# Performance work log

Measured on AMD Instinct MI355X. Metric: run time of the kernel, lower is better.

Reference implementation:

```python
import jax, jax.numpy as jnp
import numpy as np

CL = 256   # context_length (global in original code)
IL = 64    # inst_length (global in original code)
PC, CH1, CH2, CH3 = 64, 128, 256, 256
CK1, CK2, CK3 = 3, 3, 3
CS1, CS2, CS3 = 1, 2, 2
CP1, CP2, CP3 = 1, 1, 1
BCH1, BCH2, BCH3 = 64, 128, 256
F1, OUT = 1024, 2
B = 2048
C3_OUT = 64 * CH3            # 16384, per __init__ formula with CL-1=255
F1_IN = C3_OUT + BCH3        # 16640


def _conv1d(x, W, b, stride, pad):
    # x: [B, Cin, L], W: [Cout, Cin, K]
    y = jax.lax.conv_general_dilated(x, W, window_strides=(stride,),
                                     padding=[(pad, pad)],
                                     dimension_numbers=("NCH", "OIH", "NCH"))
    return y + b[None, :, None]


def setup_inputs() -> dict:
    key = jax.random.key(0)
    ks = jax.random.split(key, 20)
    s = lambda *sh: 1.0 / np.sqrt(np.prod(sh[1:]))
    def w(k, *sh):
        return jax.random.normal(k, sh, dtype=jnp.float32) * s(*sh)
    return {
        "x": jax.random.normal(ks[0], (B, CL * IL), dtype=jnp.float32),
        "Wp": w(ks[1], PC, IL, 2), "bp": jnp.zeros((PC,), jnp.float32),
        "W1": w(ks[2], CH1, PC, CK1), "b1": jnp.zeros((CH1,), jnp.float32),
        "W2": w(ks[3], CH2, CH1, CK2), "b2": jnp.zeros((CH2,), jnp.float32),
        "W3": w(ks[4], CH3, CH2, CK3), "b3": jnp.zeros((CH3,), jnp.float32),
        "Wb1": w(ks[5], BCH1, IL), "bb1": jnp.zeros((BCH1,), jnp.float32),
        "Wb2": w(ks[6], BCH2, BCH1), "bb2": jnp.zeros((BCH2,), jnp.float32),
        "Wb3": w(ks[7], BCH3, BCH2), "bb3": jnp.zeros((BCH3,), jnp.float32),
        "Wfc1": w(ks[8], F1, F1_IN), "bfc1": jnp.zeros((F1,), jnp.float32),
        "Wfc2": w(ks[9], OUT, F1), "bfc2": jnp.zeros((OUT,), jnp.float32),
    }


def reference(x, Wp, bp, W1, b1, W2, b2, W3, b3,
              Wb1, bb1, Wb2, bb2, Wb3, bb3, Wfc1, bfc1, Wfc2, bfc2):
    xr = x.reshape(-1, CL, IL).transpose(0, 2, 1)   # [B, IL, CL]
    x0 = xr[:, :, 0]                                 # [B, IL]
    # Fused replacement for the convp loop: kernel-2 conv over (x0, x_i)
    # y[:, :, i-1] = Wp[:,:,0] @ x0 + Wp[:,:,1] @ x_i + bp
    y = (jnp.einsum("bi,pi->bp", x0, Wp[:, :, 0])[:, :, None]
         + jnp.einsum("bic,pi->bpc", xr[:, :, 1:], Wp[:, :, 1])
         + bp[None, :, None])                        # [B, PC, CL-1]
    # bypass path on the first instruction (kernel-size-1 convs == matmuls)
    f = jax.nn.relu(x0 @ Wb1.T + bb1)
    f = jax.nn.relu(f @ Wb2.T + bb2)
    f = jax.nn.relu(f @ Wb3.T + bb3)                 # [B, BCH3]
    h = jax.nn.relu(y)
    h = jax.nn.relu(_conv1d(h, W1, b1, CS1, CP1))
    h = jax.nn.relu(_conv1d(h, W2, b2, CS2, CP2))
    h = jax.nn.relu(_conv1d(h, W3, b3, CS3, CP3))    # [B, CH3, 64]
    h = h.reshape(h.shape[0], C3_OUT)
    z = jnp.concatenate([h, f], axis=1)              # [B, F1_IN]
    z = jax.nn.relu(z @ Wfc1.T + bfc1)
    return z @ Wfc2.T + bfc2                         # [B, OUT]
```

## Files before the change

kernel.cpp:

```cpp
#include <hip/hip_runtime.h>
#include <cstdint>
#include <cstddef>

typedef __attribute__((ext_vector_type(8))) short bf16x8;
typedef __attribute__((ext_vector_type(8))) unsigned short ushort8;
typedef __attribute__((ext_vector_type(4))) float f32x4;

__device__ __forceinline__ unsigned short f2bf(float f){
  unsigned int u = __float_as_uint(f);
  unsigned int lsb = (u >> 16) & 1u;
  u += 0x7fffu + lsb;
  return (unsigned short)(u >> 16);
}

__device__ __forceinline__ void gload16(const void* g, void* l){
  __builtin_amdgcn_global_load_lds(
      (const __attribute__((address_space(1))) unsigned int*)g,
      (__attribute__((address_space(3))) unsigned int*)l, 16, 0, 0);
}

__global__ __launch_bounds__(256) void pack_w_bf16_kernel(const float* __restrict__ W,
                                                          unsigned short* __restrict__ Wb,
                                                          int COUT, int CIN){
  int idx = blockIdx.x*256 + threadIdx.x;
  int tot = COUT*CIN*3;
  if (idx >= tot) return;
  int o = idx/(CIN*3); int r = idx - o*(CIN*3); int kk = r/CIN; int ci = r - kk*CIN;
  Wb[idx] = f2bf(W[(o*CIN + ci)*3 + kk]);
}

__global__ __launch_bounds__(256) void pack_wp_kernel(const float* __restrict__ Wp,
                                                      unsigned short* __restrict__ Bw){
  int idx = blockIdx.x*256 + threadIdx.x;
  if (idx >= 64*128) return;
  int p = idx >> 7, k = idx & 127;
  float v = (k < 64) ? Wp[p*128 + k*2] : Wp[p*128 + (k-64)*2 + 1];
  Bw[idx] = f2bf(v);
}

__global__ __launch_bounds__(256) void f2bf_kernel(const float* __restrict__ src,
                                                   unsigned short* __restrict__ dst, int n){
  int i = blockIdx.x*256 + threadIdx.x;
  if (i < n) dst[i] = f2bf(src[i]);
}

__global__ __launch_bounds__(256) void branch_kernel(const float* __restrict__ x,
    const float* __restrict__ Wb1, const float* __restrict__ bb1,
    const float* __restrict__ Wb2, const float* __restrict__ bb2,
    const float* __restrict__ Wb3, const float* __restrict__ bb3,
    unsigned short* __restrict__ Hcat){
  __shared__ float s0[64], s1[64], s2[128];
  const int b = blockIdx.x, tid = threadIdx.x;
  const float* xb = x + (size_t)b*16384;
  if (tid < 64) s0[tid] = xb[tid];
  __syncthreads();
  if (tid < 64){
    float a = bb1[tid];
    for (int k=0;k<64;k++) a = fmaf(Wb1[tid*64+k], s0[k], a);
    s1[tid] = fmaxf(a, 0.f);
  }
  __syncthreads();
  if (tid < 128){
    float a = bb2[tid];
    for (int k=0;k<64;k++) a = fmaf(Wb2[tid*64+k], s1[k], a);
    s2[tid] = fmaxf(a, 0.f);
  }
  __syncthreads();
  float a = bb3[tid];
  for (int k=0;k<128;k++) a = fmaf(Wb3[tid*128+k], s2[k], a);
  Hcat[(size_t)b*16640 + 16384 + tid] = f2bf(fmaxf(a, 0.f));
}

__global__ __launch_bounds__(256) void h0_gemm_kernel(const float* __restrict__ x,
    const unsigned short* __restrict__ Bw, const float* __restrict__ bp,
    unsigned short* __restrict__ h0o){
  __shared__ __align__(16) char sAraw[128*256];
  __shared__ __align__(16) char sBraw[64*256];
  const int tid = threadIdx.x;
  const int m0 = blockIdx.x*128;
  #pragma unroll
  for (int i=0;i<16;i++){
    int j = tid + 256*i;
    int row = j >> 5, q = j & 31;
    int m = m0 + row;
    int b = m / 255, c = m - b*255;
    const float* xb = x + (size_t)b*16384;
    int k = q*4;
    const float* src = (k < 64) ? (xb + k) : (xb + (c+1)*64 + (k-64));
    float4 v = *(const float4*)src;
    ushort4 u; u.x=f2bf(v.x); u.y=f2bf(v.y); u.z=f2bf(v.z); u.w=f2bf(v.w);
    *(ushort4*)(sAraw + row*256 + ((k*2) ^ ((row&7)<<4))) = u;
  }
  #pragma unroll
  for (int i=0;i<4;i++){
    int j = tid + 256*i;
    int row = j >> 4, q = j & 15;
    int k = q*8;
    ushort8 u = *(const ushort8*)(Bw + row*128 + k);
    *(ushort8*)(sBraw + row*256 + ((k*2) ^ ((row&7)<<4))) = u;
  }
  __syncthreads();
  const int lane = tid & 63, wid = tid >> 6;
  const int lr = lane & 15, lg = lane >> 4;
  f32x4 zero = {0.f,0.f,0.f,0.f};
  f32x4 acc[2][4];
  #pragma unroll
  for (int a=0;a<2;a++){ acc[a][0]=zero; acc[a][1]=zero; acc[a][2]=zero; acc[a][3]=zero; }
  #pragma unroll
  for (int ks=0; ks<4; ks++){
    int k = ks*32 + lg*8;
    bf16x8 af[2], bfr[4];
    #pragma unroll
    for (int f=0; f<2; f++){
      int row = wid*32 + f*16 + lr;
      af[f] = *(const bf16x8*)(sAraw + row*256 + ((k*2) ^ ((row&7)<<4)));
    }
    #pragma unroll
    for (int f=0; f<4; f++){
      int row = f*16 + lr;
      bfr[f] = *(const bf16x8*)(sBraw + row*256 + ((k*2) ^ ((row&7)<<4)));
    }
    #pragma unroll
    for (int fi=0; fi<2; fi++)
      #pragma unroll
      for (int fj=0; fj<4; fj++)
        acc[fi][fj] = __builtin_amdgcn_mfma_f32_16x16x32_bf16(af[fi], bfr[fj], acc[fi][fj], 0,0,0);
  }
  #pragma unroll
  for (int fi=0; fi<2; fi++)
    #pragma unroll
    for (int fj=0; fj<4; fj++)
      #pragma unroll
      for (int j=0;j<4;j++){
        int m = m0 + wid*32 + fi*16 + lg*4 + j;
        int n = fj*16 + lr;
        h0o[(size_t)m*64 + n] = f2bf(fmaxf(acc[fi][fj][j] + bp[n], 0.f));
      }
}

template<int CIN,int COUT,int S,int LIN,int LOUT,int BM,int BN,int WN,bool TO_HCAT>
__global__ __launch_bounds__(256) void conv_gemm_kernel(
    const unsigned short* __restrict__ in, const unsigned short* __restrict__ Wb,
    const float* __restrict__ bias, unsigned short* __restrict__ out){
  constexpr int MT = (LOUT + BM - 1)/BM;
  __shared__ __align__(16) char sA[BM*128];
  __shared__ __align__(16) char sB[BN*128];
  const int tid = threadIdx.x;
  const int b  = blockIdx.y;
  const int mt = blockIdx.x % MT;
  const int nt = blockIdx.x / MT;
  const int m0 = mt*BM, n0 = nt*BN;
  const unsigned short* inb = in + (size_t)b*LIN*CIN;
  const int lane = tid & 63, wid = tid >> 6;
  const int wm = wid / WN, wn = wid % WN;
  const int lr = lane & 15, lg = lane >> 4;
  f32x4 zero = {0.f,0.f,0.f,0.f};
  f32x4 acc[4][4];
  #pragma unroll
  for (int i=0;i<4;i++){ acc[i][0]=zero; acc[i][1]=zero; acc[i][2]=zero; acc[i][3]=zero; }
  #pragma unroll
  for (int kk=0; kk<3; kk++){
    #pragma unroll
    for (int cc=0; cc<CIN/64; cc++){
      __syncthreads();
      #pragma unroll
      for (int p=0; p<BM/32; p++){
        int slot = tid + p*256;
        int row = slot >> 3, c8 = slot & 7;
        int pos = (m0 + row)*S - 1 + kk;
        ushort8 v = {0,0,0,0,0,0,0,0};
        if (pos >= 0 && pos < LIN)
          v = *(const ushort8*)(inb + (size_t)pos*CIN + cc*64 + c8*8);
        *(ushort8*)(sA + row*128 + ((c8*16) ^ ((row&7)<<4))) = v;
      }
      #pragma unroll
      for (int p=0; p<BN/32; p++){
        int slot = tid + p*256;
        int row = slot >> 3, c8 = slot & 7;
        ushort8 v = *(const ushort8*)(Wb + ((size_t)(n0+row)*3 + kk)*CIN + cc*64 + c8*8);
        *(ushort8*)(sB + row*128 + ((c8*16) ^ ((row&7)<<4))) = v;
      }
      __syncthreads();
      #pragma unroll
      for (int ks=0; ks<2; ks++){
        const int k = ks*32 + lg*8;
        bf16x8 af[4], bf[4];
        #pragma unroll
        for (int f=0;f<4;f++){
          int ra = wm*64 + f*16 + lr;
          af[f] = *(const bf16x8*)(sA + ra*128 + ((k*2) ^ ((ra&7)<<4)));
          int rb = wn*64 + f*16 + lr;
          bf[f] = *(const bf16x8*)(sB + rb*128 + ((k*2) ^ ((rb&7)<<4)));
        }
        #pragma unroll
        for (int fi=0;fi<4;fi++)
          #pragma unroll
          for (int fj=0;fj<4;fj++)
            acc[fi][fj] = __builtin_amdgcn_mfma_f32_16x16x32_bf16(af[fi], bf[fj], acc[fi][fj], 0,0,0);
      }
    }
  }
  unsigned short* outb = TO_HCAT ? (out + (size_t)b*16640) : (out + (size_t)b*LOUT*COUT);
  #pragma unroll
  for (int fi=0;fi<4;fi++)
    #pragma unroll
    for (int fj=0;fj<4;fj++)
      #pragma unroll
      for (int j=0;j<4;j++){
        int m = m0 + wm*64 + fi*16 + lg*4 + j;
        int n = n0 + wn*64 + fj*16 + lr;
        if (m < LOUT){
          float val = fmaxf(acc[fi][fj][j] + bias[n], 0.f);
          if (TO_HCAT) outb[(size_t)n*64 + m] = f2bf(val);
          else         outb[(size_t)m*COUT + n] = f2bf(val);
        }
      }
}

__global__ __launch_bounds__(256) void fc1_gemm_kernel(
    const unsigned short* __restrict__ A, const unsigned short* __restrict__ Bw,
    float* __restrict__ zp, int zoffm, int MT, int KZ){
  __shared__ __align__(16) char sA[128*128];
  __shared__ __align__(16) char sB[128*128];
  const int tid = threadIdx.x;
  const int nwg = gridDim.x;
  const int lgid = (blockIdx.x % 8)*(nwg/8) + blockIdx.x/8;
  const int kz  = lgid / (8*MT);
  const int rem = lgid % (8*MT);
  const int nt  = rem / MT;
  const int mt  = rem % MT;
  const int n0 = nt*128, m0 = mt*128;
  const int lane = tid & 63, wid = tid >> 6;
  const int wm = wid >> 1, wn = wid & 1;
  const int lr = lane & 15, lg = lane >> 4;
  const int srow = lane >> 3;
  const int soff = (((lane&7) ^ srow) << 3);
  f32x4 zero = {0.f,0.f,0.f,0.f};
  f32x4 acc[4][4];
  #pragma unroll
  for (int i=0;i<4;i++){ acc[i][0]=zero; acc[i][1]=zero; acc[i][2]=zero; acc[i][3]=zero; }
  const int it0 = (kz*260)/KZ, it1 = ((kz+1)*260)/KZ;
  for (int it=it0; it<it1; ++it){
    const size_t k0 = (size_t)it*64;
    __syncthreads();
    #pragma unroll
    for (int s=0;s<4;s++){
      int row = wid*32 + s*8 + srow;
      gload16(A  + (size_t)(m0+row)*16640 + k0 + soff, sA + wid*4096 + s*1024);
      gload16(Bw + (size_t)(n0+row)*16640 + k0 + soff, sB + wid*4096 + s*1024);
    }
    __syncthreads();
    #pragma unroll
    for (int ks=0; ks<2; ks++){
      const int k = ks*32 + lg*8;
      bf16x8 af[4], bfr[4];
      #pragma unroll
      for (int f=0;f<4;f++){
        int rowa = wm*64 + f*16 + lr;
        af[f]  = *(const bf16x8*)(sA + rowa*128 + ((k*2) ^ ((rowa&7)<<4)));
        int rowb = wn*64 + f*16 + lr;
        bfr[f] = *(const bf16x8*)(sB + rowb*128 + ((k*2) ^ ((rowb&7)<<4)));
      }
      #pragma unroll
      for (int fi=0;fi<4;fi++)
        #pragma unroll
        for (int fj=0;fj<4;fj++)
          acc[fi][fj] = __builtin_amdgcn_mfma_f32_16x16x32_bf16(af[fi], bfr[fj], acc[fi][fj], 0,0,0);
    }
  }
  float* zo = zp + (size_t)kz*zoffm;
  #pragma unroll
  for (int fi=0;fi<4;fi++)
    #pragma unroll
    for (int fj=0;fj<4;fj++)
      #pragma unroll
      for (int j=0;j<4;j++){
        int m = m0 + wm*64 + fi*16 + lg*4 + j;
        int n = n0 + wn*64 + fj*16 + lr;
        zo[(size_t)m*1024 + n] = acc[fi][fj][j];
      }
}

__global__ __launch_bounds__(256) void fc2_kernel(const float* __restrict__ zp, int zoffm, int KZ,
    const float* __restrict__ bfc1, const float* __restrict__ Wfc2,
    const float* __restrict__ bfc2, float* __restrict__ out){
  __shared__ float red[4][2];
  const int b = blockIdx.x, tid = threadIdx.x;
  float a0 = 0.f, a1 = 0.f;
  for (int n = tid; n < 1024; n += 256){
    float s = bfc1[n];
    const float* zb = zp + (size_t)b*1024 + n;
    for (int kz = 0; kz < KZ; kz++) s += zb[(size_t)kz*zoffm];
    s = fmaxf(s, 0.f);
    a0 = fmaf(s, Wfc2[n], a0);
    a1 = fmaf(s, Wfc2[1024+n], a1);
  }
  #pragma unroll
  for (int m=32; m>=1; m>>=1){ a0 += __shfl_xor(a0, m, 64); a1 += __shfl_xor(a1, m, 64); }
  const int w = tid >> 6;
  if ((tid & 63) == 0){ red[w][0] = a0; red[w][1] = a1; }
  __syncthreads();
  if (tid == 0){
    float s0 = red[0][0]+red[1][0]+red[2][0]+red[3][0];
    float s1 = red[0][1]+red[1][1]+red[2][1]+red[3][1];
    out[(size_t)b*2]   = s0 + bfc2[0];
    out[(size_t)b*2+1] = s1 + bfc2[1];
  }
}

extern "C" void kernel_launch(void* const* d_in, const int* in_sizes, int n_in,
                              void* d_out, int out_size, void* d_ws, size_t ws_size,
                              hipStream_t stream){
  const float* x    = (const float*)d_in[0];
  const float* Wp   = (const float*)d_in[1];
  const float* bp   = (const float*)d_in[2];
  const float* W1   = (const float*)d_in[3];
  const float* b1   = (const float*)d_in[4];
  const float* W2   = (const float*)d_in[5];
  const float* b2   = (const float*)d_in[6];
  const float* W3   = (const float*)d_in[7];
  const float* b3   = (const float*)d_in[8];
  const float* Wb1  = (const float*)d_in[9];
  const float* bb1  = (const float*)d_in[10];
  const float* Wb2  = (const float*)d_in[11];
  const float* bb2  = (const float*)d_in[12];
  const float* Wb3  = (const float*)d_in[13];
  const float* bb3  = (const float*)d_in[14];
  const float* Wfc1 = (const float*)d_in[15];
  const float* bfc1 = (const float*)d_in[16];
  const float* Wfc2 = (const float*)d_in[17];
  const float* bfc2 = (const float*)d_in[18];
  float* out = (float*)d_out;

  size_t off = 0;
  char* basep = (char*)d_ws;
  auto carve = [&](size_t bytes)->char*{
    char* q = basep + off; off += (bytes + 255) & ~(size_t)255; return q;
  };
  unsigned short* W1b   = (unsigned short*)carve((size_t)128*3*64*2);
  unsigned short* W2b   = (unsigned short*)carve((size_t)256*3*128*2);
  unsigned short* W3b   = (unsigned short*)carve((size_t)256*3*256*2);
  unsigned short* Bwp   = (unsigned short*)carve((size_t)64*128*2);
  unsigned short* Wfc1b = (unsigned short*)carve((size_t)1024*16640*2);
  size_t fixed = off;

  int Bc = 128, KZ = 64;
  {
    const int bcs[5] = {2048, 1024, 512, 256, 128};
    const int kzs[5] = {4, 8, 16, 32, 64};
    for (int i = 0; i < 5; i++){
      size_t b = bcs[i];
      size_t need = fixed + b*((size_t)65536+65280+33280) + (size_t)kzs[i]*b*4096 + 16*256;
      if (need <= ws_size){ Bc = bcs[i]; KZ = kzs[i]; break; }
    }
  }
  const int NC = 2048/Bc;
  const int MT = Bc/128;
  unsigned short* buf1 = (unsigned short*)carve((size_t)Bc*65536);
  unsigned short* buf2 = (unsigned short*)carve((size_t)Bc*65280);
  unsigned short* Hcat = (unsigned short*)carve((size_t)Bc*33280);
  float*          zp   = (float*)carve((size_t)KZ*Bc*4096);
  const int zoffm = Bc*1024;

  hipLaunchKernelGGL(pack_w_bf16_kernel, dim3((128*64*3+255)/256), dim3(256), 0, stream, W1, W1b, 128, 64);
  hipLaunchKernelGGL(pack_w_bf16_kernel, dim3((256*128*3+255)/256), dim3(256), 0, stream, W2, W2b, 256, 128);
  hipLaunchKernelGGL(pack_w_bf16_kernel, dim3((256*256*3+255)/256), dim3(256), 0, stream, W3, W3b, 256, 256);
  hipLaunchKernelGGL(pack_wp_kernel, dim3(32), dim3(256), 0, stream, Wp, Bwp);
  hipLaunchKernelGGL(f2bf_kernel, dim3((17039360+255)/256), dim3(256), 0, stream, Wfc1, Wfc1b, 17039360);

  for (int c = 0; c < NC; ++c){
    const float* xc = x + (size_t)c*Bc*16384;
    hipLaunchKernelGGL(branch_kernel, dim3(Bc), dim3(256), 0, stream,
                       xc, Wb1, bb1, Wb2, bb2, Wb3, bb3, Hcat);
    hipLaunchKernelGGL(h0_gemm_kernel, dim3(Bc*255/128), dim3(256), 0, stream, xc, Bwp, bp, buf1);
    hipLaunchKernelGGL((conv_gemm_kernel<64,128,1,255,255,128,128,2,false>), dim3(2, Bc), dim3(256), 0, stream,
                       buf1, W1b, b1, buf2);
    hipLaunchKernelGGL((conv_gemm_kernel<128,256,2,255,128,128,128,2,false>), dim3(2, Bc), dim3(256), 0, stream,
                       buf2, W2b, b2, buf1);
    hipLaunchKernelGGL((conv_gemm_kernel<256,256,2,128,64,64,256,4,true>), dim3(1, Bc), dim3(256), 0, stream,
                       buf1, W3b, b3, Hcat);
    hipLaunchKernelGGL(fc1_gemm_kernel, dim3(8*MT*KZ), dim3(256), 0, stream,
                       Hcat, Wfc1b, zp, zoffm, MT, KZ);
    hipLaunchKernelGGL(fc2_kernel, dim3(Bc), dim3(256), 0, stream,
                       zp, zoffm, KZ, bfc1, Wfc2, bfc2, out + (size_t)c*Bc*2);
  }
}
```

Measured before the change: 668.8 us.

## Pad conv activations with zero guard rows and flatten batch into GEMM M

Activation buffers gain a zero row before and after each sample, filled by a new guard-zeroing kernel, so the conv im2col loads need no bounds checks. The conv GEMM now treats batch times length as one M dimension with fixed 128x128 tiles. It stages tiles with direct global-to-LDS 16-byte loads, which removes register staging and lets tiles span sample boundaries so M=255 is no longer wasted on padding. In exchange it adds extra small kernel launches and slightly larger buffers, and it depends on the K ordering of the packed weights matching contiguous im2col rows.

```diff
diff --git a/kernel.cpp b/kernel.cpp
--- a/kernel.cpp
+++ b/kernel.cpp
@@ -42,6 +42,17 @@
                                                    unsigned short* __restrict__ dst, int n){
   int i = blockIdx.x*256 + threadIdx.x;
   if (i < n) dst[i] = f2bf(src[i]);
+}
+
+__global__ __launch_bounds__(256) void zero_guards_kernel(unsigned short* __restrict__ buf,
+                                                          int LINP, int CIN, int nb){
+  int idx = blockIdx.x*256 + threadIdx.x;
+  int per = 2*CIN/8;
+  if (idx >= nb*per) return;
+  int b = idx / per, r = idx - b*per;
+  int g = r / (CIN/8), c8 = r - g*(CIN/8);
+  ushort8 z = {0,0,0,0,0,0,0,0};
+  *(ushort8*)(buf + ((size_t)b*LINP + (size_t)g*(LINP-1))*CIN + c8*8) = z;
 }
 
 __global__ __launch_bounds__(256) void branch_kernel(const float* __restrict__ x,
@@ -134,73 +145,68 @@
       for (int j=0;j<4;j++){
         int m = m0 + wid*32 + fi*16 + lg*4 + j;
         int n = fj*16 + lr;
-        h0o[(size_t)m*64 + n] = f2bf(fmaxf(acc[fi][fj][j] + bp[n], 0.f));
-      }
-}
-
-template<int CIN,int COUT,int S,int LIN,int LOUT,int BM,int BN,int WN,bool TO_HCAT>
+        int b = m / 255, t = m - b*255;
+        h0o[((size_t)b*257 + t + 1)*64 + n] = f2bf(fmaxf(acc[fi][fj][j] + bp[n], 0.f));
+      }
+}
+
+template<int CIN,int COUT,int S,int LINP,int LOUT,bool TO_HCAT>
 __global__ __launch_bounds__(256) void conv_gemm_kernel(
     const unsigned short* __restrict__ in, const unsigned short* __restrict__ Wb,
     const float* __restrict__ bias, unsigned short* __restrict__ out){
-  constexpr int MT = (LOUT + BM - 1)/BM;
-  __shared__ __align__(16) char sA[BM*128];
-  __shared__ __align__(16) char sB[BN*128];
+  constexpr int K = 3*CIN;
+  constexpr int KS = K/64;
+  __shared__ __align__(16) char sA[128*128];
+  __shared__ __align__(16) char sB[128*128];
   const int tid = threadIdx.x;
-  const int b  = blockIdx.y;
-  const int mt = blockIdx.x % MT;
-  const int nt = blockIdx.x / MT;
-  const int m0 = mt*BM, n0 = nt*BN;
-  const unsigned short* inb = in + (size_t)b*LIN*CIN;
+  const int m0 = blockIdx.x*128;
+  const int n0 = blockIdx.y*128;
   const int lane = tid & 63, wid = tid >> 6;
-  const int wm = wid / WN, wn = wid % WN;
+  const int wm = wid >> 1, wn = wid & 1;
   const int lr = lane & 15, lg = lane >> 4;
+  const int srow = lane >> 3;
+  const int soff = (((lane&7) ^ srow) << 3);
+  const unsigned short* abase[4];
+  const unsigned short* bbase[4];
+  #pragma unroll
+  for (int s=0;s<4;s++){
+    int row = wid*32 + s*8 + srow;
+    int m = m0 + row;
+    int b = m / LOUT, t = m - b*LOUT;
+    abase[s] = in + ((size_t)b*LINP + (size_t)t*S)*CIN + soff;
+    bbase[s] = Wb + (size_t)(n0+row)*K + soff;
+  }
   f32x4 zero = {0.f,0.f,0.f,0.f};
   f32x4 acc[4][4];
   #pragma unroll
   for (int i=0;i<4;i++){ acc[i][0]=zero; acc[i][1]=zero; acc[i][2]=zero; acc[i][3]=zero; }
-  #pragma unroll
-  for (int kk=0; kk<3; kk++){
-    #pragma unroll
-    for (int cc=0; cc<CIN/64; cc++){
-      __syncthreads();
-      #pragma unroll
-      for (int p=0; p<BM/32; p++){
-        int slot = tid + p*256;
-        int row = slot >> 3, c8 = slot & 7;
-        int pos = (m0 + row)*S - 1 + kk;
-        ushort8 v = {0,0,0,0,0,0,0,0};
-        if (pos >= 0 && pos < LIN)
-          v = *(const ushort8*)(inb + (size_t)pos*CIN + cc*64 + c8*8);
-        *(ushort8*)(sA + row*128 + ((c8*16) ^ ((row&7)<<4))) = v;
-      }
-      #pragma unroll
-      for (int p=0; p<BN/32; p++){
-        int slot = tid + p*256;
-        int row = slot >> 3, c8 = slot & 7;
-        ushort8 v = *(const ushort8*)(Wb + ((size_t)(n0+row)*3 + kk)*CIN + cc*64 + c8*8);
-        *(ushort8*)(sB + row*128 + ((c8*16) ^ ((row&7)<<4))) = v;
-      }
-      __syncthreads();
-      #pragma unroll
-      for (int ks=0; ks<2; ks++){
-        const int k = ks*32 + lg*8;
-        bf16x8 af[4], bf[4];
+  for (int ks=0; ks<KS; ks++){
+    const int k0 = ks*64;
+    __syncthreads();
+    #pragma unroll
+    for (int s=0;s<4;s++){
+      gload16(abase[s] + k0, sA + wid*4096 + s*1024);
+      gload16(bbase[s] + k0, sB + wid*4096 + s*1024);
+    }
+    __syncthreads();
+    #pragma unroll
+    for (int kss=0; kss<2; kss++){
+      const int k = kss*32 + lg*8;
+      bf16x8 af[4], bfr[4];
+      #pragma unroll
+      for (int f=0;f<4;f++){
+        int ra = wm*64 + f*16 + lr;
+        af[f]  = *(const bf16x8*)(sA + ra*128 + ((k*2) ^ ((ra&7)<<4)));
+        int rb = wn*64 + f*16 + lr;
+        bfr[f] = *(const bf16x8*)(sB + rb*128 + ((k*2) ^ ((rb&7)<<4)));
+      }
+      #pragma unroll
+      for (int fi=0;fi<4;fi++)
         #pragma unroll
-        for (int f=0;f<4;f++){
-          int ra = wm*64 + f*16 + lr;
-          af[f] = *(const bf16x8*)(sA + ra*128 + ((k*2) ^ ((ra&7)<<4)));
-          int rb = wn*64 + f*16 + lr;
-          bf[f] = *(const bf16x8*)(sB + rb*128 + ((k*2) ^ ((rb&7)<<4)));
-        }
-        #pragma unroll
-        for (int fi=0;fi<4;fi++)
-          #pragma unroll
-          for (int fj=0;fj<4;fj++)
-            acc[fi][fj] = __builtin_amdgcn_mfma_f32_16x16x32_bf16(af[fi], bf[fj], acc[fi][fj], 0,0,0);
-      }
-    }
-  }
-  unsigned short* outb = TO_HCAT ? (out + (size_t)b*16640) : (out + (size_t)b*LOUT*COUT);
+        for (int fj=0;fj<4;fj++)
+          acc[fi][fj] = __builtin_amdgcn_mfma_f32_16x16x32_bf16(af[fi], bfr[fj], acc[fi][fj], 0,0,0);
+    }
+  }
   #pragma unroll
   for (int fi=0;fi<4;fi++)
     #pragma unroll
@@ -209,11 +215,10 @@
       for (int j=0;j<4;j++){
         int m = m0 + wm*64 + fi*16 + lg*4 + j;
         int n = n0 + wn*64 + fj*16 + lr;
-        if (m < LOUT){
-          float val = fmaxf(acc[fi][fj][j] + bias[n], 0.f);
-          if (TO_HCAT) outb[(size_t)n*64 + m] = f2bf(val);
-          else         outb[(size_t)m*COUT + n] = f2bf(val);
-        }
+        int b = m / LOUT, t = m - b*LOUT;
+        float val = fmaxf(acc[fi][fj][j] + bias[n], 0.f);
+        if (TO_HCAT) out[(size_t)b*16640 + (size_t)n*64 + t] = f2bf(val);
+        else         out[((size_t)b*(LOUT+2) + t + 1)*COUT + n] = f2bf(val);
       }
 }
 
@@ -350,14 +355,14 @@
     const int kzs[5] = {4, 8, 16, 32, 64};
     for (int i = 0; i < 5; i++){
       size_t b = bcs[i];
-      size_t need = fixed + b*((size_t)65536+65280+33280) + (size_t)kzs[i]*b*4096 + 16*256;
+      size_t need = fixed + b*((size_t)66560+65792+33280) + (size_t)kzs[i]*b*4096 + 16*256;
       if (need <= ws_size){ Bc = bcs[i]; KZ = kzs[i]; break; }
     }
   }
   const int NC = 2048/Bc;
   const int MT = Bc/128;
-  unsigned short* buf1 = (unsigned short*)carve((size_t)Bc*65536);
-  unsigned short* buf2 = (unsigned short*)carve((size_t)Bc*65280);
+  unsigned short* buf1 = (unsigned short*)carve((size_t)Bc*66560);
+  unsigned short* buf2 = (unsigned short*)carve((size_t)Bc*65792);
   unsigned short* Hcat = (unsigned short*)carve((size_t)Bc*33280);
   float*          zp   = (float*)carve((size_t)KZ*Bc*4096);
   const int zoffm = Bc*1024;
@@ -370,14 +375,20 @@
 
   for (int c = 0; c < NC; ++c){
     const float* xc = x + (size_t)c*Bc*16384;
+    hipLaunchKernelGGL(zero_guards_kernel, dim3((Bc*2*64/8+255)/256), dim3(256), 0, stream,
+                       buf1, 257, 64, Bc);
+    hipLaunchKernelGGL(zero_guards_kernel, dim3((Bc*2*128/8+255)/256), dim3(256), 0, stream,
+                       buf2, 257, 128, Bc);
     hipLaunchKernelGGL(branch_kernel, dim3(Bc), dim3(256), 0, stream,
                        xc, Wb1, bb1, Wb2, bb2, Wb3, bb3, Hcat);
     hipLaunchKernelGGL(h0_gemm_kernel, dim3(Bc*255/128), dim3(256), 0, stream, xc, Bwp, bp, buf1);
-    hipLaunchKernelGGL((conv_gemm_kernel<64,128,1,255,255,128,128,2,false>), dim3(2, Bc), dim3(256), 0, stream,
+    hipLaunchKernelGGL((conv_gemm_kernel<64,128,1,257,255,false>), dim3(Bc*255/128, 1), dim3(256), 0, stream,
                        buf1, W1b, b1, buf2);
-    hipLaunchKernelGGL((conv_gemm_kernel<128,256,2,255,128,128,128,2,false>), dim3(2, Bc), dim3(256), 0, stream,
+    hipLaunchKernelGGL(zero_guards_kernel, dim3((Bc*2*256/8+255)/256), dim3(256), 0, stream,
+                       buf1, 130, 256, Bc);
+    hipLaunchKernelGGL((conv_gemm_kernel<128,256,2,257,128,false>), dim3(Bc, 2), dim3(256), 0, stream,
                        buf2, W2b, b2, buf1);
-    hipLaunchKernelGGL((conv_gemm_kernel<256,256,2,128,64,64,256,4,true>), dim3(1, Bc), dim3(256), 0, stream,
+    hipLaunchKernelGGL((conv_gemm_kernel<256,256,2,130,64,true>), dim3(Bc/2, 2), dim3(256), 0, stream,
                        buf1, W3b, b3, Hcat);
     hipLaunchKernelGGL(fc1_gemm_kernel, dim3(8*MT*KZ), dim3(256), 0, stream,
                        Hcat, Wfc1b, zp, zoffm, MT, KZ);
```

Result: faster. 554.8 us (-17.1%).

## Fuse conv stages into two per-sample LDS-resident kernels

Applied to the files above, without the earlier changes.

Replaces the h0 GEMM and three separate conv GEMM launches with two per-sample kernels. fused1 computes the projection conv and conv1 entirely in shared memory. It also factors out the x0 term into a per-sample bias, so the K dimension is halved. fused2 keeps conv1 output and conv2 output in LDS to compute conv2 and conv3, with register-prefetched weight tiles. This cuts global round-trips of intermediate activations and the number of launches. The cost is very large LDS footprints (~115KB and ~154KB), which limit occupancy to one block per CU, and weights are reloaded per sample.

```diff
diff --git a/kernel.cpp b/kernel.cpp
--- a/kernel.cpp
+++ b/kernel.cpp
@@ -13,6 +13,11 @@
   return (unsigned short)(u >> 16);
 }
 
+__device__ __forceinline__ ushort8 cvt8(const float4 a, const float4 b){
+  ushort8 u; u[0]=f2bf(a.x); u[1]=f2bf(a.y); u[2]=f2bf(a.z); u[3]=f2bf(a.w);
+  u[4]=f2bf(b.x); u[5]=f2bf(b.y); u[6]=f2bf(b.z); u[7]=f2bf(b.w); return u;
+}
+
 __device__ __forceinline__ void gload16(const void* g, void* l){
   __builtin_amdgcn_global_load_lds(
       (const __attribute__((address_space(1))) unsigned int*)g,
@@ -20,8 +25,7 @@
 }
 
 __global__ __launch_bounds__(256) void pack_w_bf16_kernel(const float* __restrict__ W,
-                                                          unsigned short* __restrict__ Wb,
-                                                          int COUT, int CIN){
+    unsigned short* __restrict__ Wb, int COUT, int CIN){
   int idx = blockIdx.x*256 + threadIdx.x;
   int tot = COUT*CIN*3;
   if (idx >= tot) return;
@@ -29,13 +33,12 @@
   Wb[idx] = f2bf(W[(o*CIN + ci)*3 + kk]);
 }
 
-__global__ __launch_bounds__(256) void pack_wp_kernel(const float* __restrict__ Wp,
-                                                      unsigned short* __restrict__ Bw){
+__global__ __launch_bounds__(256) void pack_bh_kernel(const float* __restrict__ Wp,
+                                                      unsigned short* __restrict__ Bh){
   int idx = blockIdx.x*256 + threadIdx.x;
-  if (idx >= 64*128) return;
-  int p = idx >> 7, k = idx & 127;
-  float v = (k < 64) ? Wp[p*128 + k*2] : Wp[p*128 + (k-64)*2 + 1];
-  Bw[idx] = f2bf(v);
+  if (idx >= 64*64) return;
+  int p = idx >> 6, i = idx & 63;
+  Bh[idx] = f2bf(Wp[p*128 + i*2 + 1]);
 }
 
 __global__ __launch_bounds__(256) void f2bf_kernel(const float* __restrict__ src,
@@ -71,150 +74,297 @@
   Hcat[(size_t)b*16640 + 16384 + tid] = f2bf(fmaxf(a, 0.f));
 }
 
-__global__ __launch_bounds__(256) void h0_gemm_kernel(const float* __restrict__ x,
-    const unsigned short* __restrict__ Bw, const float* __restrict__ bp,
-    unsigned short* __restrict__ h0o){
-  __shared__ __align__(16) char sAraw[128*256];
-  __shared__ __align__(16) char sBraw[64*256];
-  const int tid = threadIdx.x;
-  const int m0 = blockIdx.x*128;
-  #pragma unroll
-  for (int i=0;i<16;i++){
-    int j = tid + 256*i;
-    int row = j >> 5, q = j & 31;
-    int m = m0 + row;
-    int b = m / 255, c = m - b*255;
-    const float* xb = x + (size_t)b*16384;
-    int k = q*4;
-    const float* src = (k < 64) ? (xb + k) : (xb + (c+1)*64 + (k-64));
-    float4 v = *(const float4*)src;
-    ushort4 u; u.x=f2bf(v.x); u.y=f2bf(v.y); u.z=f2bf(v.z); u.w=f2bf(v.w);
-    *(ushort4*)(sAraw + row*256 + ((k*2) ^ ((row&7)<<4))) = u;
-  }
+__global__ __launch_bounds__(512) void fused1_kernel(
+    const float* __restrict__ x, const float* __restrict__ Wp, const float* __restrict__ bp,
+    const unsigned short* __restrict__ Bh, const unsigned short* __restrict__ W1b,
+    const float* __restrict__ b1, unsigned short* __restrict__ c1g){
+  __shared__ __align__(16) char S[115392];
+  constexpr int SX = 0;
+  constexpr int SH = 37008;
+  constexpr int SB = 74160;
+  constexpr int SW = 106928;
+  constexpr int SY = 115120;
+  const int b = blockIdx.x, tid = threadIdx.x;
+  const int lane = tid & 63, wv = tid >> 6;
+  const int lr = lane & 15, lg = lane >> 4;
+  const float* xg = x + (size_t)b*16384;
+
   #pragma unroll
   for (int i=0;i<4;i++){
-    int j = tid + 256*i;
-    int row = j >> 4, q = j & 15;
-    int k = q*8;
-    ushort8 u = *(const ushort8*)(Bw + row*128 + k);
-    *(ushort8*)(sBraw + row*256 + ((k*2) ^ ((row&7)<<4))) = u;
+    int s = tid + 512*i;
+    int row = s>>3, sl = s&7;
+    const float4* src = (const float4*)(xg + row*64 + sl*8);
+    *(ushort8*)(S + SX + row*144 + sl*16) = cvt8(src[0], src[1]);
+  }
+  { int row = tid>>3, sl = tid&7;
+    ushort8 u = *(const ushort8*)(Bh + row*64 + sl*8);
+    *(ushort8*)(S + SW + row*128 + ((sl*16)^((row&7)<<4))) = u; }
+  ushort8 z8 = {0,0,0,0,0,0,0,0};
+  if (tid < 9)        *(ushort8*)(S + SX + 256*144 + tid*16) = z8;
+  else if (tid < 18)  *(ushort8*)(S + SH + 0*144   + (tid-9)*16) = z8;
+  else if (tid < 27)  *(ushort8*)(S + SH + 257*144 + (tid-18)*16) = z8;
+  if (tid < 64){
+    float a = bp[tid];
+    const float* wr = Wp + tid*128;
+    #pragma unroll 8
+    for (int i=0;i<64;i++) a = fmaf(wr[2*i], xg[i], a);
+    *(float*)(S + SY + tid*4) = a;
   }
   __syncthreads();
-  const int lane = tid & 63, wid = tid >> 6;
-  const int lr = lane & 15, lg = lane >> 4;
-  f32x4 zero = {0.f,0.f,0.f,0.f};
-  f32x4 acc[2][4];
-  #pragma unroll
-  for (int a=0;a<2;a++){ acc[a][0]=zero; acc[a][1]=zero; acc[a][2]=zero; acc[a][3]=zero; }
-  #pragma unroll
-  for (int ks=0; ks<4; ks++){
-    int k = ks*32 + lg*8;
-    bf16x8 af[2], bfr[4];
-    #pragma unroll
-    for (int f=0; f<2; f++){
-      int row = wid*32 + f*16 + lr;
-      af[f] = *(const bf16x8*)(sAraw + row*256 + ((k*2) ^ ((row&7)<<4)));
-    }
-    #pragma unroll
-    for (int f=0; f<4; f++){
-      int row = f*16 + lr;
-      bfr[f] = *(const bf16x8*)(sBraw + row*256 + ((k*2) ^ ((row&7)<<4)));
-    }
-    #pragma unroll
-    for (int fi=0; fi<2; fi++)
-      #pragma unroll
-      for (int fj=0; fj<4; fj++)
-        acc[fi][fj] = __builtin_amdgcn_mfma_f32_16x16x32_bf16(af[fi], bfr[fj], acc[fi][fj], 0,0,0);
-  }
-  #pragma unroll
-  for (int fi=0; fi<2; fi++)
-    #pragma unroll
-    for (int fj=0; fj<4; fj++)
-      #pragma unroll
-      for (int j=0;j<4;j++){
-        int m = m0 + wid*32 + fi*16 + lg*4 + j;
-        int n = fj*16 + lr;
-        h0o[(size_t)m*64 + n] = f2bf(fmaxf(acc[fi][fj][j] + bp[n], 0.f));
+
+  {
+    const int wm = wv>>1, wn = wv&1;
+    f32x4 acc[4][2];
+    #pragma unroll
+    for (int i=0;i<4;i++){ acc[i][0]=(f32x4){0,0,0,0}; acc[i][1]=(f32x4){0,0,0,0}; }
+    #pragma unroll
+    for (int ks=0; ks<2; ks++){
+      int k = ks*32 + lg*8;
+      bf16x8 af[4], bf[2];
+      #pragma unroll
+      for (int f=0;f<4;f++){ int ar = wm*64 + f*16 + lr + 1;
+        af[f] = *(const bf16x8*)(S + SX + ar*144 + k*2); }
+      #pragma unroll
+      for (int f=0;f<2;f++){ int rb = wn*32 + f*16 + lr;
+        bf[f] = *(const bf16x8*)(S + SW + rb*128 + ((k*2)^((rb&7)<<4))); }
+      #pragma unroll
+      for (int i=0;i<4;i++)
+        #pragma unroll
+        for (int j=0;j<2;j++)
+          acc[i][j] = __builtin_amdgcn_mfma_f32_16x16x32_bf16(af[i], bf[j], acc[i][j], 0,0,0);
+    }
+    #pragma unroll
+    for (int fm=0;fm<4;fm++)
+      #pragma unroll
+      for (int fn=0;fn<2;fn++)
+        #pragma unroll
+        for (int j=0;j<4;j++){
+          int t = wm*64 + fm*16 + lg*4 + j;
+          int p = wn*32 + fn*16 + lr;
+          float v = acc[fm][fn][j] + *(const float*)(S + SY + p*4);
+          unsigned short o = (t < 255) ? f2bf(fmaxf(v, 0.f)) : (unsigned short)0;
+          *(unsigned short*)(S + SH + (t+1)*144 + p*2) = o;
+        }
+  }
+
+  {
+    const int soff = ((lane&7)^(lane>>3))<<3;
+    const int rbase = wv*8 + (lane>>3);
+    #pragma unroll
+    for (int s=0;s<2;s++)
+      gload16(W1b + (size_t)(s*64 + rbase)*192 + soff, S + SB + s*8192 + wv*1024);
+    __syncthreads();
+
+    const int wm = wv>>1, wn = wv&1;
+    f32x4 acc[4][4];
+    #pragma unroll
+    for (int i=0;i<4;i++)
+      #pragma unroll
+      for (int j=0;j<4;j++) acc[i][j] = (f32x4){0,0,0,0};
+    #pragma unroll
+    for (int c=0;c<3;c++){
+      int buf = c&1;
+      if (c<2){
+        #pragma unroll
+        for (int s=0;s<2;s++)
+          gload16(W1b + (size_t)(s*64 + rbase)*192 + (c+1)*64 + soff,
+                  S + SB + (buf^1)*16384 + s*8192 + wv*1024);
       }
-}
-
-template<int CIN,int COUT,int S,int LIN,int LOUT,int BM,int BN,int WN,bool TO_HCAT>
-__global__ __launch_bounds__(256) void conv_gemm_kernel(
-    const unsigned short* __restrict__ in, const unsigned short* __restrict__ Wb,
-    const float* __restrict__ bias, unsigned short* __restrict__ out){
-  constexpr int MT = (LOUT + BM - 1)/BM;
-  __shared__ __align__(16) char sA[BM*128];
-  __shared__ __align__(16) char sB[BN*128];
-  const int tid = threadIdx.x;
-  const int b  = blockIdx.y;
-  const int mt = blockIdx.x % MT;
-  const int nt = blockIdx.x / MT;
-  const int m0 = mt*BM, n0 = nt*BN;
-  const unsigned short* inb = in + (size_t)b*LIN*CIN;
-  const int lane = tid & 63, wid = tid >> 6;
-  const int wm = wid / WN, wn = wid % WN;
-  const int lr = lane & 15, lg = lane >> 4;
-  f32x4 zero = {0.f,0.f,0.f,0.f};
-  f32x4 acc[4][4];
-  #pragma unroll
-  for (int i=0;i<4;i++){ acc[i][0]=zero; acc[i][1]=zero; acc[i][2]=zero; acc[i][3]=zero; }
-  #pragma unroll
-  for (int kk=0; kk<3; kk++){
-    #pragma unroll
-    for (int cc=0; cc<CIN/64; cc++){
-      __syncthreads();
-      #pragma unroll
-      for (int p=0; p<BM/32; p++){
-        int slot = tid + p*256;
-        int row = slot >> 3, c8 = slot & 7;
-        int pos = (m0 + row)*S - 1 + kk;
-        ushort8 v = {0,0,0,0,0,0,0,0};
-        if (pos >= 0 && pos < LIN)
-          v = *(const ushort8*)(inb + (size_t)pos*CIN + cc*64 + c8*8);
-        *(ushort8*)(sA + row*128 + ((c8*16) ^ ((row&7)<<4))) = v;
-      }
-      #pragma unroll
-      for (int p=0; p<BN/32; p++){
-        int slot = tid + p*256;
-        int row = slot >> 3, c8 = slot & 7;
-        ushort8 v = *(const ushort8*)(Wb + ((size_t)(n0+row)*3 + kk)*CIN + cc*64 + c8*8);
-        *(ushort8*)(sB + row*128 + ((c8*16) ^ ((row&7)<<4))) = v;
+      #pragma unroll
+      for (int ks=0; ks<2; ks++){
+        int k = ks*32 + lg*8;
+        bf16x8 af[4], bf[4];
+        #pragma unroll
+        for (int f=0;f<4;f++){ int ar = wm*64 + f*16 + lr + c;
+          af[f] = *(const bf16x8*)(S + SH + ar*144 + k*2); }
+        #pragma unroll
+        for (int f=0;f<4;f++){ int rb = wn*64 + f*16 + lr;
+          bf[f] = *(const bf16x8*)(S + SB + buf*16384 + rb*128 + ((k*2)^((rb&7)<<4))); }
+        #pragma unroll
+        for (int i=0;i<4;i++)
+          #pragma unroll
+          for (int j=0;j<4;j++)
+            acc[i][j] = __builtin_amdgcn_mfma_f32_16x16x32_bf16(af[i], bf[j], acc[i][j], 0,0,0);
       }
       __syncthreads();
-      #pragma unroll
-      for (int ks=0; ks<2; ks++){
-        const int k = ks*32 + lg*8;
-        bf16x8 af[4], bf[4];
-        #pragma unroll
-        for (int f=0;f<4;f++){
-          int ra = wm*64 + f*16 + lr;
-          af[f] = *(const bf16x8*)(sA + ra*128 + ((k*2) ^ ((ra&7)<<4)));
-          int rb = wn*64 + f*16 + lr;
-          bf[f] = *(const bf16x8*)(sB + rb*128 + ((k*2) ^ ((rb&7)<<4)));
+    }
+    unsigned short* cbo = c1g + (size_t)b*32640;
+    #pragma unroll
+    for (int fi=0;fi<4;fi++)
+      #pragma unroll
+      for (int fj=0;fj<4;fj++)
+        #pragma unroll
+        for (int j=0;j<4;j++){
+          int t = wm*64 + fi*16 + lg*4 + j;
+          int n = wn*64 + fj*16 + lr;
+          if (t < 255) cbo[(size_t)t*128 + n] = f2bf(fmaxf(acc[fi][fj][j] + b1[n], 0.f));
         }
-        #pragma unroll
-        for (int fi=0;fi<4;fi++)
+  }
+}
+
+__device__ __forceinline__ void ldb512(const unsigned short* __restrict__ W, int rowstride,
+                                       int n0, int kbase, int tid, ushort8* breg){
+  #pragma unroll
+  for (int h=0; h<2; h++){
+    int s = tid + 512*h, row = s>>3, sl = s&7;
+    breg[h] = *(const ushort8*)(W + (size_t)(n0+row)*rowstride + kbase + sl*8);
+  }
+}
+__device__ __forceinline__ void stb512(char* Sb, int tid, const ushort8* breg){
+  #pragma unroll
+  for (int h=0; h<2; h++){
+    int s = tid + 512*h, row = s>>3, sl = s&7;
+    *(ushort8*)(Sb + row*128 + ((sl*16)^((row&7)<<4))) = breg[h];
+  }
+}
+
+__global__ __launch_bounds__(512) void fused2_kernel(
+    const unsigned short* __restrict__ c1g, const unsigned short* __restrict__ W2b,
+    const float* __restrict__ b2, const unsigned short* __restrict__ W3b,
+    const float* __restrict__ b3, unsigned short* __restrict__ Hcat){
+  __shared__ __align__(16) char S[154400];
+  constexpr int SC1 = 0;
+  constexpr int SC2 = 69904;
+  constexpr int SB  = 138016;
+  const int b = blockIdx.x, tid = threadIdx.x;
+  const int lane = tid & 63, wv = tid >> 6;
+  const int lr = lane & 15, lg = lane >> 4;
+  const unsigned short* cbi = c1g + (size_t)b*32640;
+
+  ushort8 bA[2], bB[2];
+  ldb512(W2b, 384, 0, 0, tid, bA);
+
+  #pragma unroll
+  for (int i=0;i<8;i++){
+    int s = tid + 512*i;
+    if (s < 4080){
+      int row = s>>4, sl = s&15;
+      ushort8 u = *(const ushort8*)(cbi + (size_t)row*128 + sl*8);
+      *(ushort8*)(S + SC1 + (row+1)*272 + sl*16) = u;
+    }
+  }
+  ushort8 z8 = {0,0,0,0,0,0,0,0};
+  if (tid < 17)       *(ushort8*)(S + SC1 + 0       + tid*16) = z8;
+  else if (tid < 34)  *(ushort8*)(S + SC1 + 256*272 + (tid-17)*16) = z8;
+  else if (tid < 67)  *(ushort8*)(S + SC2 + 0       + (tid-34)*16) = z8;
+
+  {
+    const int wm = wv>>1, wn = wv&1;
+    #pragma unroll
+    for (int np=0; np<2; np++){
+      f32x4 acc[2][4];
+      #pragma unroll
+      for (int i=0;i<2;i++)
+        #pragma unroll
+        for (int j=0;j<4;j++) acc[i][j] = (f32x4){0,0,0,0};
+      #pragma unroll
+      for (int c2=0; c2<3; c2++){
+        #pragma unroll
+        for (int half=0; half<2; half++){
+          const int c = 2*c2 + half;
+          __syncthreads();
+          stb512(S + SB, tid, half ? bB : bA);
+          __syncthreads();
+          if (half == 0){
+            int cn = c + 1;
+            ldb512(W2b, 384, np*128, (cn>>1)*128 + (cn&1)*64, tid, bB);
+          } else if (c2 < 2){
+            int cn = c + 1;
+            ldb512(W2b, 384, np*128, (cn>>1)*128 + (cn&1)*64, tid, bA);
+          } else if (np == 0){
+            ldb512(W2b, 384, 128, 0, tid, bA);
+          } else {
+            ldb512(W3b, 768, 0, 0, tid, bA);
+          }
+          const int kk = c>>1, ch = (c&1)*64;
           #pragma unroll
-          for (int fj=0;fj<4;fj++)
-            acc[fi][fj] = __builtin_amdgcn_mfma_f32_16x16x32_bf16(af[fi], bf[fj], acc[fi][fj], 0,0,0);
-      }
-    }
-  }
-  unsigned short* outb = TO_HCAT ? (out + (size_t)b*16640) : (out + (size_t)b*LOUT*COUT);
-  #pragma unroll
-  for (int fi=0;fi<4;fi++)
-    #pragma unroll
-    for (int fj=0;fj<4;fj++)
-      #pragma unroll
-      for (int j=0;j<4;j++){
-        int m = m0 + wm*64 + fi*16 + lg*4 + j;
-        int n = n0 + wn*64 + fj*16 + lr;
-        if (m < LOUT){
-          float val = fmaxf(acc[fi][fj][j] + bias[n], 0.f);
-          if (TO_HCAT) outb[(size_t)n*64 + m] = f2bf(val);
-          else         outb[(size_t)m*COUT + n] = f2bf(val);
+          for (int ks=0; ks<2; ks++){
+            int kp = ks*32 + lg*8;
+            bf16x8 af[2], bf[4];
+            #pragma unroll
+            for (int f=0;f<2;f++){ int ar = 2*(wm*32 + f*16 + lr) + kk;
+              af[f] = *(const bf16x8*)(S + SC1 + ar*272 + (ch+kp)*2); }
+            #pragma unroll
+            for (int f=0;f<4;f++){ int rb = wn*64 + f*16 + lr;
+              bf[f] = *(const bf16x8*)(S + SB + rb*128 + ((kp*2)^((rb&7)<<4))); }
+            #pragma unroll
+            for (int i=0;i<2;i++)
+              #pragma unroll
+              for (int j=0;j<4;j++)
+                acc[i][j] = __builtin_amdgcn_mfma_f32_16x16x32_bf16(af[i], bf[j], acc[i][j], 0,0,0);
+          }
         }
       }
+      #pragma unroll
+      for (int fm=0;fm<2;fm++)
+        #pragma unroll
+        for (int fn=0;fn<4;fn++)
+          #pragma unroll
+          for (int j=0;j<4;j++){
+            int t = wm*32 + fm*16 + lg*4 + j;
+            int n = np*128 + wn*64 + fn*16 + lr;
+            *(unsigned short*)(S + SC2 + (t+1)*528 + n*2) =
+                f2bf(fmaxf(acc[fm][fn][j] + b2[n], 0.f));
+          }
+    }
+  }
+
+  {
+    const int wm = wv>>2, wn = wv&3;
+    #pragma unroll
+    for (int np=0; np<2; np++){
+      f32x4 acc[2][2];
+      #pragma unroll
+      for (int i=0;i<2;i++){ acc[i][0]=(f32x4){0,0,0,0}; acc[i][1]=(f32x4){0,0,0,0}; }
+      #pragma unroll
+      for (int c2=0; c2<6; c2++){
+        #pragma unroll
+        for (int half=0; half<2; half++){
+          const int c = 2*c2 + half;
+          __syncthreads();
+          stb512(S + SB, tid, half ? bB : bA);
+          __syncthreads();
+          if (half == 0){
+            int cn = c + 1;
+            ldb512(W3b, 768, np*128, (cn>>2)*256 + (cn&3)*64, tid, bB);
+          } else if (c2 < 5){
+            int cn = c + 1;
+            ldb512(W3b, 768, np*128, (cn>>2)*256 + (cn&3)*64, tid, bA);
+          } else if (np == 0){
+            ldb512(W3b, 768, 128, 0, tid, bA);
+          }
+          const int kk = c>>2, q = c&3;
+          #pragma unroll
+          for (int ks=0; ks<2; ks++){
+            int kp = ks*32 + lg*8;
+            bf16x8 af[2], bf[2];
+            #pragma unroll
+            for (int f=0;f<2;f++){ int ar = 2*(wm*32 + f*16 + lr) + kk;
+              af[f] = *(const bf16x8*)(S + SC2 + ar*528 + (q*64+kp)*2); }
+            #pragma unroll
+            for (int f=0;f<2;f++){ int rb = wn*32 + f*16 + lr;
+              bf[f] = *(const bf16x8*)(S + SB + rb*128 + ((kp*2)^((rb&7)<<4))); }
+            #pragma unroll
+            for (int i=0;i<2;i++)
+              #pragma unroll
+              for (int j=0;j<2;j++)
+                acc[i][j] = __builtin_amdgcn_mfma_f32_16x16x32_bf16(af[i], bf[j], acc[i][j], 0,0,0);
+          }
+        }
+      }
+      unsigned short* hb = Hcat + (size_t)b*16640;
+      #pragma unroll
+      for (int fm=0;fm<2;fm++)
+        #pragma unroll
+        for (int fn=0;fn<2;fn++)
+          #pragma unroll
+          for (int j=0;j<4;j++){
+            int t = wm*32 + fm*16 + lg*4 + j;
+            int n = np*128 + wn*32 + fn*16 + lr;
+            hb[(size_t)n*64 + t] = f2bf(fmaxf(acc[fm][fn][j] + b3[n], 0.f));
+          }
+    }
+  }
 }
 
 __global__ __launch_bounds__(256) void fc1_gemm_kernel(
@@ -301,10 +451,8 @@
   if ((tid & 63) == 0){ red[w][0] = a0; red[w][1] = a1; }
   __syncthreads();
   if (tid == 0){
-    float s0 = red[0][0]+red[1][0]+red[2][0]+red[3][0];
-    float s1 = red[0][1]+red[1][1]+red[2][1]+red[3][1];
-    out[(size_t)b*2]   = s0 + bfc2[0];
-    out[(size_t)b*2+1] = s1 + bfc2[1];
+    out[(size_t)b*2]   = red[0][0]+red[1][0]+red[2][0]+red[3][0] + bfc2[0];
+    out[(size_t)b*2+1] = red[0][1]+red[1][1]+red[2][1]+red[3][1] + bfc2[1];
   }
 }
 
@@ -340,7 +488,7 @@
   unsigned short* W1b   = (unsigned short*)carve((size_t)128*3*64*2);
   unsigned short* W2b   = (unsigned short*)carve((size_t)256*3*128*2);
   unsigned short* W3b   = (unsigned short*)carve((size_t)256*3*256*2);
-  unsigned short* Bwp   = (unsigned short*)carve((size_t)64*128*2);
+  unsigned short* Bhp   = (unsigned short*)carve((size_t)64*64*2);
   unsigned short* Wfc1b = (unsigned short*)carve((size_t)1024*16640*2);
   size_t fixed = off;
 
@@ -349,15 +497,14 @@
     const int bcs[5] = {2048, 1024, 512, 256, 128};
     const int kzs[5] = {4, 8, 16, 32, 64};
     for (int i = 0; i < 5; i++){
-      size_t b = bcs[i];
-      size_t need = fixed + b*((size_t)65536+65280+33280) + (size_t)kzs[i]*b*4096 + 16*256;
+      size_t bsz = bcs[i];
+      size_t need = fixed + bsz*((size_t)65280+33280) + (size_t)kzs[i]*bsz*4096 + 16*256;
       if (need <= ws_size){ Bc = bcs[i]; KZ = kzs[i]; break; }
     }
   }
   const int NC = 2048/Bc;
   const int MT = Bc/128;
-  unsigned short* buf1 = (unsigned short*)carve((size_t)Bc*65536);
-  unsigned short* buf2 = (unsigned short*)carve((size_t)Bc*65280);
+  unsigned short* c1g  = (unsigned short*)carve((size_t)Bc*65280);
   unsigned short* Hcat = (unsigned short*)carve((size_t)Bc*33280);
   float*          zp   = (float*)carve((size_t)KZ*Bc*4096);
   const int zoffm = Bc*1024;
@@ -365,20 +512,17 @@
   hipLaunchKernelGGL(pack_w_bf16_kernel, dim3((128*64*3+255)/256), dim3(256), 0, stream, W1, W1b, 128, 64);
   hipLaunchKernelGGL(pack_w_bf16_kernel, dim3((256*128*3+255)/256), dim3(256), 0, stream, W2, W2b, 256, 128);
   hipLaunchKernelGGL(pack_w_bf16_kernel, dim3((256*256*3+255)/256), dim3(256), 0, stream, W3, W3b, 256, 256);
-  hipLaunchKernelGGL(pack_wp_kernel, dim3(32), dim3(256), 0, stream, Wp, Bwp);
+  hipLaunchKernelGGL(pack_bh_kernel, dim3(16), dim3(256), 0, stream, Wp, Bhp);
   hipLaunchKernelGGL(f2bf_kernel, dim3((17039360+255)/256), dim3(256), 0, stream, Wfc1, Wfc1b, 17039360);
 
   for (int c = 0; c < NC; ++c){
     const float* xc = x + (size_t)c*Bc*16384;
     hipLaunchKernelGGL(branch_kernel, dim3(Bc), dim3(256), 0, stream,
                        xc, Wb1, bb1, Wb2, bb2, Wb3, bb3, Hcat);
-    hipLaunchKernelGGL(h0_gemm_kernel, dim3(Bc*255/128), dim3(256), 0, stream, xc, Bwp, bp, buf1);
-    hipLaunchKernelGGL((conv_gemm_kernel<64,128,1,255,255,128,128,2,false>), dim3(2, Bc), dim3(256), 0, stream,
-                       buf1, W1b, b1, buf2);
-    hipLaunchKernelGGL((conv_gemm_kernel<128,256,2,255,128,128,128,2,false>), dim3(2, Bc), dim3(256), 0, stream,
-                       buf2, W2b, b2, buf1);
-    hipLaunchKernelGGL((conv_gemm_kernel<256,256,2,128,64,64,256,4,true>), dim3(1, Bc), dim3(256), 0, stream,
-                       buf1, W3b, b3, Hcat);
+    hipLaunchKernelGGL(fused1_kernel, dim3(Bc), dim3(512), 0, stream,
+                       xc, Wp, bp, Bhp, W1b, b1, c1g);
+    hipLaunchKernelGGL(fused2_kernel, dim3(Bc), dim3(512), 0, stream,
+                       c1g, W2b, b2, W3b, b3, Hcat);
     hipLaunchKernelGGL(fc1_gemm_kernel, dim3(8*MT*KZ), dim3(256), 0, stream,
                        Hcat, Wfc1b, zp, zoffm, MT, KZ);
     hipLaunchKernelGGL(fc2_kernel, dim3(Bc), dim3(256), 0, stream,
```

Measured after the change: 574.2 us. 14.1% less time.
